# Performance work log

Measured on AMD Instinct MI355X. Metric: run time of the kernel, lower is better.

Reference implementation:

```python
import jax, jax.numpy as jnp
import numpy as np

B, L, D = 8, 2048, 1024
NH = 16            # n_head
HD = D // NH       # 64; attention is (HD x HD) per token in this module


def setup_inputs() -> dict:
    key = jax.random.key(0)
    ks = jax.random.split(key, 5)
    s = 0.02  # init scale for weights
    return {
        "x": jax.random.normal(ks[0], (B, L, D), jnp.float32),
        "Wq": jax.random.normal(ks[1], (D, D), jnp.float32) * s,
        "bq": jnp.zeros((D,), jnp.float32),
        "Wk": jax.random.normal(ks[2], (D, D), jnp.float32) * s,
        "bk": jnp.zeros((D,), jnp.float32),
        "Wv": jax.random.normal(ks[3], (D, D), jnp.float32) * s,
        "bv": jnp.zeros((D,), jnp.float32),
        "Wo": jax.random.normal(ks[4], (D, D), jnp.float32) * s,
        "bo": jnp.zeros((D,), jnp.float32),
    }


def reference(x, Wq, bq, Wk, bk, Wv, bv, Wo, bo):
    b, l, d = x.shape
    # QKV projections
    q = (x @ Wq + bq).reshape(b, l, HD, NH)
    k = (x @ Wk + bk).reshape(b, l, HD, NH)
    v = (x @ Wv + bv).reshape(b, l, HD, NH)
    # NOTE: module reshapes to (b, l, head_dim, n_head), so scores are
    # per-token (HD, HD) with the NH axis contracted; norm = sqrt(NH).
    norm = jnp.sqrt(jnp.asarray(NH, x.dtype))
    attn = jnp.einsum('blij,blkj->blik', q, k) / norm  # (b, l, HD, HD)
    attn = attn + 1e-06
    # mask = tril of the VALUES; jnp.where uses nonzero-as-True semantics.
    mask = jnp.tril(attn)
    attn = jnp.where(mask, attn, -jnp.inf)
    probs = jax.nn.softmax(attn, axis=-1)
    y = jnp.einsum('blik,blkj->blij', probs, v).reshape(b, l, d)
    return y @ Wo + bo
```

## Files before the change

### kernel.cpp

```cpp
#include <hip/hip_runtime.h>
#include <hip/hip_bf16.h>
#include <stdint.h>

typedef unsigned short u16;

#define Bdim 8
#define Ldim 2048
#define Ddim 1024
#define NH 16
#define HD 64
#define MTOK (Bdim*Ldim)

typedef __bf16 bf16x8 __attribute__((ext_vector_type(8)));
typedef float  f32x4  __attribute__((ext_vector_type(4)));
typedef float  f32x16 __attribute__((ext_vector_type(16)));

#define AS1 __attribute__((address_space(1)))
#define AS3 __attribute__((address_space(3)))

__device__ __forceinline__ void gload_lds16(const void* g, void* l) {
  __builtin_amdgcn_global_load_lds((const AS1 void*)g, (AS3 void*)l, 16, 0, 0);
}

__device__ __forceinline__ u16 f2bf(float f) {
  uint32_t u = __builtin_bit_cast(uint32_t, f);
  u += 0x7fffu + ((u >> 16) & 1u);
  return (u16)(u >> 16);
}
__device__ __forceinline__ uint32_t pkpair(float lo, float hi) {
  return (uint32_t)f2bf(lo) | ((uint32_t)f2bf(hi) << 16);
}

__global__ __launch_bounds__(256) void conv_f32_bf16(const float* __restrict__ in,
                                                     u16* __restrict__ out, int n4) {
  int i = blockIdx.x * 256 + threadIdx.x;
  if (i < n4) {
    float4 v = ((const float4*)in)[i];
    uint32_t w0 = (uint32_t)f2bf(v.x) | ((uint32_t)f2bf(v.y) << 16);
    uint32_t w1 = (uint32_t)f2bf(v.z) | ((uint32_t)f2bf(v.w) << 16);
    ((uint2*)out)[i] = make_uint2(w0, w1);
  }
}

__global__ __launch_bounds__(256) void conv_transpose_w(const float* __restrict__ W,
                                                        u16* __restrict__ Wt) {
  __shared__ float t[32][33];
  int tx = threadIdx.x & 31, ty = threadIdx.x >> 5;
  int k0 = blockIdx.x * 32, n0 = blockIdx.y * 32;
  #pragma unroll
  for (int i = 0; i < 32; i += 8)
    t[ty + i][tx] = W[(size_t)(k0 + ty + i) * Ddim + n0 + tx];
  __syncthreads();
  #pragma unroll
  for (int i = 0; i < 32; i += 8)
    Wt[(size_t)(n0 + ty + i) * Ddim + k0 + tx] = f2bf(t[tx][ty + i]);
}

template <int FUSED>
__global__ __launch_bounds__(512, 2) void gemm256(const u16* __restrict__ A,
                                                  const u16* __restrict__ Bt,
                                                  const float* __restrict__ b0p,
                                                  const float* __restrict__ b1p,
                                                  const float* __restrict__ b2p,
                                                  void* __restrict__ o0,
                                                  void* __restrict__ o1,
                                                  void* __restrict__ o2) {
  __shared__ alignas(16) u16 LP[65536];
  u16* LA = LP;
  u16* LB = LP + 32768;

  const int tid = threadIdx.x;
  const int wid = tid >> 6, lane = tid & 63;
  const int wr = wid >> 2, wc = wid & 3;
  const int fr = lane & 15, fh = lane >> 4;
  const int key = fr & 7;

  const int bid = blockIdx.x;
  const int xcd = bid & 7, idx = bid >> 3;
  const int mt = xcd * 8 + (idx & 7);
  const int nt = idx >> 3;
  const int m0 = mt * 256;
  const int n0g = nt * 256;

  const int srow = wid * 8 + (lane >> 3);
  const int scol = ((lane & 7) ^ (lane >> 3)) * 8;
  const u16* aG = A  + (size_t)(m0  + srow) * 1024 + scol;
  const u16* bG = Bt + (size_t)(n0g + srow) * 1024 + scol;
  const int ldsW = wid * 512;

#define STAGE(tile, buf) do {                                                  \
    const u16* ag_ = aG + (size_t)(tile) * 64;                                  \
    const u16* bg_ = bG + (size_t)(tile) * 64;                                  \
    _Pragma("unroll")                                                           \
    for (int s_ = 0; s_ < 4; ++s_) {                                            \
      gload_lds16(ag_ + (size_t)s_ * 65536, LA + (buf) * 16384 + s_ * 4096 + ldsW); \
      gload_lds16(bg_ + (size_t)s_ * 65536, LB + (buf) * 16384 + s_ * 4096 + ldsW); \
    }                                                                           \
  } while (0)

  f32x4 acc[8][4] = {};

#define COMPUTE(buf) do {                                                       \
    _Pragma("unroll")                                                           \
    for (int ks_ = 0; ks_ < 2; ++ks_) {                                         \
      bf16x8 af_[8], bf_[4];                                                    \
      const int p_ = ((ks_ * 4 + fh) ^ key) * 8;                                \
      _Pragma("unroll")                                                         \
      for (int m_ = 0; m_ < 8; ++m_)                                            \
        af_[m_] = *(const bf16x8*)(LA + (buf) * 16384 +                         \
                                   (wr * 128 + m_ * 16 + fr) * 64 + p_);        \
      _Pragma("unroll")                                                         \
      for (int n_ = 0; n_ < 4; ++n_)                                            \
        bf_[n_] = *(const bf16x8*)(LB + (buf) * 16384 +                         \
                                   (wc * 64 + n_ * 16 + fr) * 64 + p_);         \
      __builtin_amdgcn_s_setprio(1);                                            \
      _Pragma("unroll")                                                         \
      for (int m_ = 0; m_ < 8; ++m_)                                            \
        _Pragma("unroll")                                                       \
        for (int n_ = 0; n_ < 4; ++n_)                                          \
          acc[m_][n_] = __builtin_amdgcn_mfma_f32_16x16x32_bf16(                \
              af_[m_], bf_[n_], acc[m_][n_], 0, 0, 0);                          \
      __builtin_amdgcn_s_setprio(0);                                            \
    }                                                                           \
  } while (0)

  STAGE(0, 0);
  #pragma unroll 1
  for (int t = 0; t < 15; ++t) {
    const int cur = t & 1;
    STAGE(t + 1, cur ^ 1);
    asm volatile("s_waitcnt vmcnt(8)" ::: "memory");
    __builtin_amdgcn_s_barrier();
    COMPUTE(cur);
    asm volatile("s_waitcnt lgkmcnt(0)" ::: "memory");
    __builtin_amdgcn_s_barrier();
  }
  asm volatile("s_waitcnt vmcnt(0)" ::: "memory");
  __builtin_amdgcn_s_barrier();
  COMPUTE(1);
  __syncthreads();

  if (FUSED) {
    const int which = nt >> 2;
    const int n0l = (nt & 3) * 256;
    const float* bias = which == 0 ? b0p : which == 1 ? b1p : b2p;
    u16* Out = (u16*)(which == 0 ? o0 : which == 1 ? o1 : o2);
    u16* Ct = LP;
    #pragma unroll 1
    for (int h = 0; h < 2; ++h) {
      if (h) __syncthreads();
      if (wr == h) {
        #pragma unroll
        for (int n = 0; n < 4; ++n) {
          float bvv = bias[n0l + wc * 64 + n * 16 + fr];
          #pragma unroll
          for (int m = 0; m < 8; ++m)
            #pragma unroll
            for (int r = 0; r < 4; ++r)
              Ct[wc * 9216 + (m * 16 + fh * 4 + r) * 72 + n * 16 + fr] =
                  f2bf(acc[m][n][r] + bvv);
        }
      }
      __syncthreads();
      if (which != 2) {
        #pragma unroll
        for (int j = 0; j < 8; ++j) {
          int r = j * 16 + (tid >> 5), c8 = tid & 31;
          uint4 v = *(const uint4*)(Ct + (c8 >> 3) * 9216 + r * 72 + (c8 & 7) * 8);
          *(uint4*)(Out + (size_t)(m0 + h * 128 + r) * Ddim + n0l + c8 * 8) = v;
        }
      } else {
        #pragma unroll
        for (int j = 0; j < 4; ++j) {
          int q = j * 512 + tid, r = q >> 4, i = q & 15;
          u16 tmp[16];
          #pragma unroll
          for (int jj = 0; jj < 16; ++jj) {
            int c = i + 16 * jj;
            tmp[jj] = Ct[(c >> 6) * 9216 + r * 72 + (c & 63)];
          }
          u16* dst = Out + (size_t)(m0 + h * 128 + r) * Ddim + i * 64 + (n0l >> 4);
          *(uint4*)dst = *(uint4*)tmp;
          *(uint4*)(dst + 8) = *(uint4*)(tmp + 8);
        }
      }
      __syncthreads();
    }
  } else {
    float* Cf = (float*)LP;
    float* Out = (float*)o0;
    #pragma unroll 1
    for (int h = 0; h < 4; ++h) {
      if (h) __syncthreads();
      if (wr == (h >> 1) && (wc >> 1) == (h & 1)) {
        #pragma unroll
        for (int n = 0; n < 4; ++n) {
          int col = (wc & 1) * 64 + n * 16 + fr;
          float bvv = b0p[n0g + (h & 1) * 128 + col];
          #pragma unroll
          for (int m = 0; m < 8; ++m)
            #pragma unroll
            for (int r = 0; r < 4; ++r)
              Cf[(wc & 1) * 8704 + (m * 16 + fh * 4 + r) * 68 + n * 16 + fr] =
                  acc[m][n][r] + bvv;
        }
      }
      __syncthreads();
      #pragma unroll
      for (int j = 0; j < 8; ++j) {
        int r = j * 16 + (tid >> 5), c4 = tid & 31;
        float4 v = *(const float4*)(Cf + (c4 >> 4) * 8704 + r * 68 + (c4 & 15) * 4);
        *(float4*)(Out + (size_t)(m0 + (h >> 1) * 128 + r) * Ddim +
                   n0g + (h & 1) * 128 + c4 * 4) = v;
      }
      __syncthreads();
    }
  }
#undef STAGE
#undef COMPUTE
}

__global__ __launch_bounds__(256) void attn_mfma(const u16* __restrict__ Q,
                                                 const u16* __restrict__ Kb,
                                                 const u16* __restrict__ Vt,
                                                 u16* __restrict__ Y) {
  const int wid = threadIdx.x >> 6, lane = threadIdx.x & 63;
  const int tok = blockIdx.x * 4 + wid;
  const size_t base = (size_t)tok * Ddim;
  const int hi = lane >> 5, c31 = lane & 31;

  const bf16x8 kf0 = *(const bf16x8*)(Kb + base + (size_t)c31 * NH + hi * 8);
  const bf16x8 kf1 = *(const bf16x8*)(Kb + base + (size_t)(32 + c31) * NH + hi * 8);
  const bf16x8 qf0 = *(const bf16x8*)(Q  + base + (size_t)c31 * NH + hi * 8);
  const bf16x8 qf1 = *(const bf16x8*)(Q  + base + (size_t)(32 + c31) * NH + hi * 8);
  bf16x8 bv[4];
  #pragma unroll
  for (int c = 0; c < 4; ++c)
    bv[c] = *(const bf16x8*)(Vt + base + (size_t)(lane & 15) * HD + c * 16 + hi * 8);

  const f32x16 z = {};
  f32x16 s00 = __builtin_amdgcn_mfma_f32_32x32x16_bf16(kf0, qf0, z, 0, 0, 0);
  f32x16 s01 = __builtin_amdgcn_mfma_f32_32x32x16_bf16(kf0, qf1, z, 0, 0, 0);
  f32x16 s11 = __builtin_amdgcn_mfma_f32_32x32x16_bf16(kf1, qf1, z, 0, 0, 0);

  float a[16], b0[16], b1[16];
  float mA = -3e38f, mB = -3e38f;
  #pragma unroll
  for (int r = 0; r < 16; ++r) {
    const int kl = (r & 3) + 8 * (r >> 2) + 4 * hi;
    const bool keep = kl <= c31;
    float v00 = fmaf(s00[r], 0.25f, 1e-6f);
    float v01 = fmaf(s01[r], 0.25f, 1e-6f);
    float v11 = fmaf(s11[r], 0.25f, 1e-6f);
    a[r]  = keep ? v00 : -3e38f;
    b0[r] = v01;
    b1[r] = keep ? v11 : -3e38f;
    mA = fmaxf(mA, a[r]);
    mB = fmaxf(mB, fmaxf(b0[r], b1[r]));
  }
  mA = fmaxf(mA, __shfl_xor(mA, 32, 64));
  mB = fmaxf(mB, __shfl_xor(mB, 32, 64));
  float sA = 0.f, sB = 0.f;
  #pragma unroll
  for (int r = 0; r < 16; ++r) {
    a[r]  = __expf(a[r]  - mA);  sA += a[r];
    b0[r] = __expf(b0[r] - mB);
    b1[r] = __expf(b1[r] - mB);  sB += b0[r] + b1[r];
  }
  sA += __shfl_xor(sA, 32, 64);
  sB += __shfl_xor(sB, 32, 64);
  const float iA = __builtin_amdgcn_rcpf(sA);
  const float iB = __builtin_amdgcn_rcpf(sB);

  uint32_t pA[4][2], pB0[4][2], pB1[4][2];
  #pragma unroll
  for (int m = 0; m < 4; ++m)
    #pragma unroll
    for (int t = 0; t < 2; ++t) {
      pA [m][t] = pkpair(a [4*m+2*t] * iA, a [4*m+2*t+1] * iA);
      pB0[m][t] = pkpair(b0[4*m+2*t] * iB, b0[4*m+2*t+1] * iB);
      pB1[m][t] = pkpair(b1[4*m+2*t] * iB, b1[4*m+2*t+1] * iB);
    }

#define AFRAG(dst, src, cp) do {                                              \
    uint32_t k0_ = hi ? src[2*(cp)+1][0] : src[2*(cp)][0];                    \
    uint32_t k1_ = hi ? src[2*(cp)+1][1] : src[2*(cp)][1];                    \
    uint32_t s0_ = hi ? src[2*(cp)][0]   : src[2*(cp)+1][0];                  \
    uint32_t s1_ = hi ? src[2*(cp)][1]   : src[2*(cp)+1][1];                  \
    uint32_t r0_ = (uint32_t)__shfl_xor((int)s0_, 32, 64);                    \
    uint32_t r1_ = (uint32_t)__shfl_xor((int)s1_, 32, 64);                    \
    union { uint32_t w[4]; bf16x8 v; } u_;                                    \
    u_.w[0] = hi ? r0_ : k0_;  u_.w[1] = hi ? r1_ : k1_;                      \
    u_.w[2] = hi ? k0_ : r0_;  u_.w[3] = hi ? k1_ : r1_;                      \
    dst = u_.v;                                                               \
  } while (0)

  f32x16 y0 = {}, y1 = {};
  bf16x8 af;
  AFRAG(af, pA, 0);  y0 = __builtin_amdgcn_mfma_f32_32x32x16_bf16(af, bv[0], y0, 0, 0, 0);
  AFRAG(af, pA, 1);  y0 = __builtin_amdgcn_mfma_f32_32x32x16_bf16(af, bv[1], y0, 0, 0, 0);
  AFRAG(af, pB0, 0); y1 = __builtin_amdgcn_mfma_f32_32x32x16_bf16(af, bv[0], y1, 0, 0, 0);
  AFRAG(af, pB0, 1); y1 = __builtin_amdgcn_mfma_f32_32x32x16_bf16(af, bv[1], y1, 0, 0, 0);
  AFRAG(af, pB1, 0); y1 = __builtin_amdgcn_mfma_f32_32x32x16_bf16(af, bv[2], y1, 0, 0, 0);
  AFRAG(af, pB1, 1); y1 = __builtin_amdgcn_mfma_f32_32x32x16_bf16(af, bv[3], y1, 0, 0, 0);
#undef AFRAG

  if (c31 < 16) {
    #pragma unroll
    for (int r = 0; r < 16; ++r) {
      const int row = (r & 3) + 8 * (r >> 2) + 4 * hi;
      Y[base + (size_t)row * NH + c31]        = f2bf(y0[r]);
      Y[base + (size_t)(32 + row) * NH + c31] = f2bf(y1[r]);
    }
  }
}

extern "C" void kernel_launch(void* const* d_in, const int* in_sizes, int n_in,
                              void* d_out, int out_size, void* d_ws, size_t ws_size,
                              hipStream_t stream) {
  const float* x  = (const float*)d_in[0];
  const float* Wq = (const float*)d_in[1];
  const float* bq = (const float*)d_in[2];
  const float* Wk = (const float*)d_in[3];
  const float* bk = (const float*)d_in[4];
  const float* Wv = (const float*)d_in[5];
  const float* bv = (const float*)d_in[6];
  const float* Wo = (const float*)d_in[7];
  const float* bo = (const float*)d_in[8];
  float* out = (float*)d_out;

  u16* xb = (u16*)d_ws;
  u16* Wt = xb + (size_t)MTOK * Ddim;
  u16* Qb = Wt + 4ull * Ddim * Ddim;
  u16* Kb = Qb + (size_t)MTOK * Ddim;
  u16* Vb = Kb + (size_t)MTOK * Ddim;
  u16* Yb = xb;

  conv_f32_bf16<<<(MTOK * Ddim / 4 + 255) / 256, 256, 0, stream>>>(x, xb, MTOK * Ddim / 4);

  dim3 tg(Ddim / 32, Ddim / 32);
  conv_transpose_w<<<tg, 256, 0, stream>>>(Wq, Wt + 0ull * Ddim * Ddim);
  conv_transpose_w<<<tg, 256, 0, stream>>>(Wk, Wt + 1ull * Ddim * Ddim);
  conv_transpose_w<<<tg, 256, 0, stream>>>(Wv, Wt + 2ull * Ddim * Ddim);
  conv_transpose_w<<<tg, 256, 0, stream>>>(Wo, Wt + 3ull * Ddim * Ddim);

  gemm256<1><<<dim3(768), 512, 0, stream>>>(xb, Wt, bq, bk, bv, Qb, Kb, Vb);

  attn_mfma<<<MTOK / 4, 256, 0, stream>>>(Qb, Kb, Vb, Yb);

  gemm256<0><<<dim3(256), 512, 0, stream>>>(Yb, Wt + 3ull * Ddim * Ddim,
                                            bo, bo, bo, out, out, out);
}
```

Baseline: 213.3 us.

## Interleave global-to-LDS loads, LDS fragment reads and MFMAs in GEMM main loop

Restructures the GEMM K-loop into four quarter-steps that alternate between two register fragment sets. Each quarter-step issues part of the next tile's global-to-LDS loads, prefetches LDS fragments for the next MFMA group and runs 16 MFMAs, so loads, LDS reads and matrix math overlap within a tile. The old version ran a full stage-wait-compute-barrier cycle per tile. The new schedule adds more barriers and finer vmcnt waits, and it raises register pressure from the extra fragment buffers.

```diff
diff --git a/kernel.cpp b/kernel.cpp
--- a/kernel.cpp
+++ b/kernel.cpp
@@ -88,56 +88,75 @@
   const u16* bG = Bt + (size_t)(n0g + srow) * 1024 + scol;
   const int ldsW = wid * 512;
 
-#define STAGE(tile, buf) do {                                                  \
-    const u16* ag_ = aG + (size_t)(tile) * 64;                                  \
-    const u16* bg_ = bG + (size_t)(tile) * 64;                                  \
+#define STG(MAT, S_, TILE, BUF)                                                 \
+  gload_lds16(((MAT) ? bG : aG) + (size_t)(TILE) * 64 + (size_t)(S_) * 65536,   \
+              ((MAT) ? LB : LA) + (BUF) * 16384 + (S_) * 4096 + ldsW)
+
+#define RD_AF(DST, BUF, KS, MH) do {                                            \
+    const u16* base_ = LA + (BUF) * 16384;                                      \
+    const int p_ = (((KS) * 4 + fh) ^ key) * 8;                                 \
     _Pragma("unroll")                                                           \
-    for (int s_ = 0; s_ < 4; ++s_) {                                            \
-      gload_lds16(ag_ + (size_t)s_ * 65536, LA + (buf) * 16384 + s_ * 4096 + ldsW); \
-      gload_lds16(bg_ + (size_t)s_ * 65536, LB + (buf) * 16384 + s_ * 4096 + ldsW); \
-    }                                                                           \
+    for (int mm_ = 0; mm_ < 4; ++mm_)                                           \
+      DST[mm_] = *(const bf16x8*)(base_ +                                       \
+                   (wr * 128 + (MH) * 64 + mm_ * 16 + fr) * 64 + p_);           \
   } while (0)
-
-  f32x4 acc[8][4] = {};
-
-#define COMPUTE(buf) do {                                                       \
+#define RD_BF(DST, BUF, KS) do {                                                \
+    const u16* base_ = LB + (BUF) * 16384;                                      \
+    const int p_ = (((KS) * 4 + fh) ^ key) * 8;                                 \
     _Pragma("unroll")                                                           \
-    for (int ks_ = 0; ks_ < 2; ++ks_) {                                         \
-      bf16x8 af_[8], bf_[4];                                                    \
-      const int p_ = ((ks_ * 4 + fh) ^ key) * 8;                                \
-      _Pragma("unroll")                                                         \
-      for (int m_ = 0; m_ < 8; ++m_)                                            \
-        af_[m_] = *(const bf16x8*)(LA + (buf) * 16384 +                         \
-                                   (wr * 128 + m_ * 16 + fr) * 64 + p_);        \
+    for (int n_ = 0; n_ < 4; ++n_)                                              \
+      DST[n_] = *(const bf16x8*)(base_ + (wc * 64 + n_ * 16 + fr) * 64 + p_);   \
+  } while (0)
+#define MFMA16(AF, BF, MH) do {                                                 \
+    __builtin_amdgcn_s_setprio(1);                                              \
+    _Pragma("unroll")                                                           \
+    for (int mm_ = 0; mm_ < 4; ++mm_)                                           \
       _Pragma("unroll")                                                         \
       for (int n_ = 0; n_ < 4; ++n_)                                            \
-        bf_[n_] = *(const bf16x8*)(LB + (buf) * 16384 +                         \
-                                   (wc * 64 + n_ * 16 + fr) * 64 + p_);         \
-      __builtin_amdgcn_s_setprio(1);                                            \
-      _Pragma("unroll")                                                         \
-      for (int m_ = 0; m_ < 8; ++m_)                                            \
-        _Pragma("unroll")                                                       \
-        for (int n_ = 0; n_ < 4; ++n_)                                          \
-          acc[m_][n_] = __builtin_amdgcn_mfma_f32_16x16x32_bf16(                \
-              af_[m_], bf_[n_], acc[m_][n_], 0, 0, 0);                          \
-      __builtin_amdgcn_s_setprio(0);                                            \
-    }                                                                           \
+        acc[(MH) * 4 + mm_][n_] = __builtin_amdgcn_mfma_f32_16x16x32_bf16(      \
+            AF[mm_], BF[n_], acc[(MH) * 4 + mm_][n_], 0, 0, 0);                 \
+    __builtin_amdgcn_s_setprio(0);                                              \
   } while (0)
-
-  STAGE(0, 0);
+#define WAITV(N) asm volatile("s_waitcnt vmcnt(" #N ")" ::: "memory")
+#define BAR() __builtin_amdgcn_s_barrier()
+
+  f32x4 acc[8][4] = {};
+  bf16x8 afA[4], afB[4], bf0[4], bf1[4];
+
+  STG(1,0,0,0); STG(1,1,0,0); STG(1,2,0,0); STG(1,3,0,0);
+  STG(0,0,0,0); STG(0,2,0,0); STG(0,1,0,0); STG(0,3,0,0);
+  WAITV(2); BAR();
+  RD_AF(afA, 0, 0, 0); RD_BF(bf0, 0, 0);
+
   #pragma unroll 1
   for (int t = 0; t < 15; ++t) {
-    const int cur = t & 1;
-    STAGE(t + 1, cur ^ 1);
-    asm volatile("s_waitcnt vmcnt(8)" ::: "memory");
-    __builtin_amdgcn_s_barrier();
-    COMPUTE(cur);
-    asm volatile("s_waitcnt lgkmcnt(0)" ::: "memory");
-    __builtin_amdgcn_s_barrier();
-  }
-  asm volatile("s_waitcnt vmcnt(0)" ::: "memory");
-  __builtin_amdgcn_s_barrier();
-  COMPUTE(1);
+    const int cur = t & 1, nxt = cur ^ 1;
+    STG(1,0,t+1,nxt); STG(1,1,t+1,nxt);
+    BAR();
+    RD_AF(afB, cur, 1, 0); RD_BF(bf1, cur, 1);
+    MFMA16(afA, bf0, 0);
+    STG(1,2,t+1,nxt); STG(1,3,t+1,nxt);
+    WAITV(4); BAR();
+    RD_AF(afA, cur, 0, 1);
+    MFMA16(afB, bf1, 0);
+    STG(0,0,t+1,nxt); STG(0,2,t+1,nxt);
+    BAR();
+    RD_AF(afB, cur, 1, 1);
+    MFMA16(afA, bf0, 1);
+    STG(0,1,t+1,nxt); STG(0,3,t+1,nxt);
+    WAITV(2); BAR();
+    RD_AF(afA, nxt, 0, 0); RD_BF(bf0, nxt, 0);
+    MFMA16(afB, bf1, 1);
+  }
+  RD_AF(afB, 1, 1, 0); RD_BF(bf1, 1, 1);
+  MFMA16(afA, bf0, 0);
+  WAITV(0); BAR();
+  RD_AF(afA, 1, 0, 1);
+  MFMA16(afB, bf1, 0);
+  RD_AF(afB, 1, 1, 1);
+  MFMA16(afA, bf0, 1);
+  MFMA16(afB, bf1, 1);
+
   __syncthreads();
 
   if (FUSED) {
@@ -195,8 +214,7 @@
       if (wr == (h >> 1) && (wc >> 1) == (h & 1)) {
         #pragma unroll
         for (int n = 0; n < 4; ++n) {
-          int col = (wc & 1) * 64 + n * 16 + fr;
-          float bvv = b0p[n0g + (h & 1) * 128 + col];
+          float bvv = b0p[n0g + (h & 1) * 128 + (wc & 1) * 64 + n * 16 + fr];
           #pragma unroll
           for (int m = 0; m < 8; ++m)
             #pragma unroll
@@ -216,8 +234,12 @@
       __syncthreads();
     }
   }
-#undef STAGE
-#undef COMPUTE
+#undef STG
+#undef RD_AF
+#undef RD_BF
+#undef MFMA16
+#undef WAITV
+#undef BAR
 }
 
 __global__ __launch_bounds__(256) void attn_mfma(const u16* __restrict__ Q,
```

Measured after the change: 206.9 us. 1.03x faster.

## Restructure GEMM main loop into 8-phase interleaved load/compute pipeline

Applied to the files above, without the earlier changes.

Replaces the double-buffered stage/compute loop in the bf16 GEMM with an 8-phase schedule. Each phase splits the tile into half-tiles, interleaves LDS fragment reads, global-to-LDS half-tile loads and a 16-MFMA cluster, and puts barriers between them. The aim is to hide LDS read latency and global load latency behind MFMA work, in the style of ping-pong GEMM schedules. It adds many more barriers and fine-grained vmcnt waits, so correctness depends on the hand-tracked buffer and ordering logic.

```diff
diff --git a/kernel.cpp b/kernel.cpp
--- a/kernel.cpp
+++ b/kernel.cpp
@@ -57,87 +57,103 @@
 }
 
 template <int FUSED>
-__global__ __launch_bounds__(512, 2) void gemm256(const u16* __restrict__ A,
-                                                  const u16* __restrict__ Bt,
-                                                  const float* __restrict__ b0p,
-                                                  const float* __restrict__ b1p,
-                                                  const float* __restrict__ b2p,
-                                                  void* __restrict__ o0,
-                                                  void* __restrict__ o1,
-                                                  void* __restrict__ o2) {
+__global__ __launch_bounds__(512, 2) void gemm8p(const u16* __restrict__ A,
+                                                 const u16* __restrict__ Bt,
+                                                 const float* __restrict__ b0p,
+                                                 const float* __restrict__ b1p,
+                                                 const float* __restrict__ b2p,
+                                                 void* __restrict__ o0,
+                                                 void* __restrict__ o1,
+                                                 void* __restrict__ o2) {
   __shared__ alignas(16) u16 LP[65536];
-  u16* LA = LP;
-  u16* LB = LP + 32768;
-
   const int tid = threadIdx.x;
   const int wid = tid >> 6, lane = tid & 63;
   const int wr = wid >> 2, wc = wid & 3;
   const int fr = lane & 15, fh = lane >> 4;
-  const int key = fr & 7;
 
   const int bid = blockIdx.x;
   const int xcd = bid & 7, idx = bid >> 3;
   const int mt = xcd * 8 + (idx & 7);
   const int nt = idx >> 3;
-  const int m0 = mt * 256;
-  const int n0g = nt * 256;
-
-  const int srow = wid * 8 + (lane >> 3);
-  const int scol = ((lane & 7) ^ (lane >> 3)) * 8;
-  const u16* aG = A  + (size_t)(m0  + srow) * 1024 + scol;
-  const u16* bG = Bt + (size_t)(n0g + srow) * 1024 + scol;
-  const int ldsW = wid * 512;
-
-#define STAGE(tile, buf) do {                                                  \
-    const u16* ag_ = aG + (size_t)(tile) * 64;                                  \
-    const u16* bg_ = bG + (size_t)(tile) * 64;                                  \
-    _Pragma("unroll")                                                           \
-    for (int s_ = 0; s_ < 4; ++s_) {                                            \
-      gload_lds16(ag_ + (size_t)s_ * 65536, LA + (buf) * 16384 + s_ * 4096 + ldsW); \
-      gload_lds16(bg_ + (size_t)s_ * 65536, LB + (buf) * 16384 + s_ * 4096 + ldsW); \
-    }                                                                           \
-  } while (0)
+  const int m0 = mt * 256, n0g = nt * 256;
+
+  const int x7 = fr & 7;
+  const int cks0 = (fh ^ x7) * 8;
+  const int cks1 = ((4 + fh) ^ x7) * 8;
+  const int rA = (wr * 128 + fr) * 64;
+  const int rB = (wc * 64 + fr) * 64;
+
+  const int srt = tid >> 3;
+  const int sgc = ((tid & 7) ^ (srt & 7)) * 8;
+  const u16* aSt = A  + (size_t)(m0  + srt) * 1024 + sgc;
+  const u16* bSt = Bt + (size_t)(n0g + srt) * 1024 + sgc;
+
+#define RDA4(DST, B_, KS_, MH_) do {                                           \
+    const u16* p_ = LP + (B_) * 16384 + rA + (MH_) * 4096 + ((KS_) ? cks1 : cks0); \
+    DST[0] = *(const bf16x8*)(p_);                                             \
+    DST[1] = *(const bf16x8*)(p_ + 1024);                                      \
+    DST[2] = *(const bf16x8*)(p_ + 2048);                                      \
+    DST[3] = *(const bf16x8*)(p_ + 3072);                                      \
+  } while (0)
+#define RDB4(DST, B_, KS_) do {                                                \
+    const u16* p_ = LP + 32768 + (B_) * 16384 + rB + ((KS_) ? cks1 : cks0);    \
+    DST[0] = *(const bf16x8*)(p_);                                             \
+    DST[1] = *(const bf16x8*)(p_ + 1024);                                      \
+    DST[2] = *(const bf16x8*)(p_ + 2048);                                      \
+    DST[3] = *(const bf16x8*)(p_ + 3072);                                      \
+  } while (0)
+#define STGH(ISB_, T_, H_, B_) do {                                            \
+    const u16* s_ = ((ISB_) ? bSt : aSt) + (size_t)(H_) * 131072 + (size_t)(T_) * 64; \
+    u16* d_ = (u16*)LP + ((ISB_) ? 32768 : 0) + (B_) * 16384 + (H_) * 8192 + (wid << 9); \
+    gload_lds16(s_, d_);                                                       \
+    gload_lds16(s_ + 65536, d_ + 4096);                                        \
+  } while (0)
+#define MFMA16(AF, BF, MH) do {                                                \
+    __builtin_amdgcn_s_setprio(1);                                             \
+    _Pragma("unroll")                                                          \
+    for (int mm_ = 0; mm_ < 4; ++mm_)                                          \
+      _Pragma("unroll")                                                        \
+      for (int n_ = 0; n_ < 4; ++n_)                                           \
+        acc[(MH) * 4 + mm_][n_] = __builtin_amdgcn_mfma_f32_16x16x32_bf16(     \
+            AF[mm_], BF[n_], acc[(MH) * 4 + mm_][n_], 0, 0, 0);                \
+    __builtin_amdgcn_s_setprio(0);                                             \
+  } while (0)
+#define WAITV(N) asm volatile("s_waitcnt vmcnt(" #N ")" ::: "memory")
+#define BAR() do { asm volatile("" ::: "memory");                              \
+                   __builtin_amdgcn_s_barrier();                               \
+                   asm volatile("" ::: "memory"); } while (0)
 
   f32x4 acc[8][4] = {};
-
-#define COMPUTE(buf) do {                                                       \
-    _Pragma("unroll")                                                           \
-    for (int ks_ = 0; ks_ < 2; ++ks_) {                                         \
-      bf16x8 af_[8], bf_[4];                                                    \
-      const int p_ = ((ks_ * 4 + fh) ^ key) * 8;                                \
-      _Pragma("unroll")                                                         \
-      for (int m_ = 0; m_ < 8; ++m_)                                            \
-        af_[m_] = *(const bf16x8*)(LA + (buf) * 16384 +                         \
-                                   (wr * 128 + m_ * 16 + fr) * 64 + p_);        \
-      _Pragma("unroll")                                                         \
-      for (int n_ = 0; n_ < 4; ++n_)                                            \
-        bf_[n_] = *(const bf16x8*)(LB + (buf) * 16384 +                         \
-                                   (wc * 64 + n_ * 16 + fr) * 64 + p_);         \
-      __builtin_amdgcn_s_setprio(1);                                            \
-      _Pragma("unroll")                                                         \
-      for (int m_ = 0; m_ < 8; ++m_)                                            \
-        _Pragma("unroll")                                                       \
-        for (int n_ = 0; n_ < 4; ++n_)                                          \
-          acc[m_][n_] = __builtin_amdgcn_mfma_f32_16x16x32_bf16(                \
-              af_[m_], bf_[n_], acc[m_][n_], 0, 0, 0);                          \
-      __builtin_amdgcn_s_setprio(0);                                            \
-    }                                                                           \
-  } while (0)
-
-  STAGE(0, 0);
+  bf16x8 aA[4], aB[4], bA[4], bB[4];
+
+  STGH(1, 0, 0, 0); STGH(0, 0, 0, 0); STGH(1, 0, 1, 0); STGH(0, 0, 1, 0);
+  STGH(1, 1, 0, 1); STGH(0, 1, 0, 1);
+  WAITV(4);
+  BAR();
+  RDA4(aA, 0, 0, 0); RDB4(bA, 0, 0);
+
   #pragma unroll 1
-  for (int t = 0; t < 15; ++t) {
-    const int cur = t & 1;
-    STAGE(t + 1, cur ^ 1);
-    asm volatile("s_waitcnt vmcnt(8)" ::: "memory");
-    __builtin_amdgcn_s_barrier();
-    COMPUTE(cur);
-    asm volatile("s_waitcnt lgkmcnt(0)" ::: "memory");
-    __builtin_amdgcn_s_barrier();
-  }
-  asm volatile("s_waitcnt vmcnt(0)" ::: "memory");
-  __builtin_amdgcn_s_barrier();
-  COMPUTE(1);
+  for (int i = 0; i < 8; ++i) {
+    const int u1 = 2 * i + 1;
+    const int s2 = (i < 7) ? 2 * i + 2 : 14;
+    const int s3 = (i < 7) ? 2 * i + 3 : 15;
+    RDA4(aB, 0, 0, 1);                 STGH(1, u1, 1, 1);
+    BAR(); MFMA16(aA, bA, 0); BAR();
+    RDA4(aA, 0, 1, 0); RDB4(bB, 0, 1); STGH(0, u1, 1, 1);
+    BAR(); MFMA16(aB, bA, 1); BAR();
+    RDA4(aB, 0, 1, 1);                 STGH(1, s2, 0, 0);
+    BAR(); MFMA16(aA, bB, 0); WAITV(2); BAR();
+    RDA4(aA, 1, 0, 0); RDB4(bA, 1, 0); STGH(0, s2, 0, 0);
+    BAR(); MFMA16(aB, bB, 1); BAR();
+    RDA4(aB, 1, 0, 1);                 STGH(1, s2, 1, 0);
+    BAR(); MFMA16(aA, bA, 0); BAR();
+    RDA4(aA, 1, 1, 0); RDB4(bB, 1, 1); STGH(0, s2, 1, 0);
+    BAR(); MFMA16(aB, bA, 1); BAR();
+    RDA4(aB, 1, 1, 1);                 STGH(1, s3, 0, 1);
+    BAR(); MFMA16(aA, bB, 0); WAITV(2); BAR();
+    RDA4(aA, 0, 0, 0); RDB4(bA, 0, 0); STGH(0, s3, 0, 1);
+    BAR(); MFMA16(aB, bB, 1); BAR();
+  }
   __syncthreads();
 
   if (FUSED) {
@@ -172,14 +188,14 @@
       } else {
         #pragma unroll
         for (int j = 0; j < 4; ++j) {
-          int q = j * 512 + tid, r = q >> 4, i = q & 15;
+          int q = j * 512 + tid, r = q >> 4, ii = q & 15;
           u16 tmp[16];
           #pragma unroll
           for (int jj = 0; jj < 16; ++jj) {
-            int c = i + 16 * jj;
+            int c = ii + 16 * jj;
             tmp[jj] = Ct[(c >> 6) * 9216 + r * 72 + (c & 63)];
           }
-          u16* dst = Out + (size_t)(m0 + h * 128 + r) * Ddim + i * 64 + (n0l >> 4);
+          u16* dst = Out + (size_t)(m0 + h * 128 + r) * Ddim + ii * 64 + (n0l >> 4);
           *(uint4*)dst = *(uint4*)tmp;
           *(uint4*)(dst + 8) = *(uint4*)(tmp + 8);
         }
@@ -195,8 +211,7 @@
       if (wr == (h >> 1) && (wc >> 1) == (h & 1)) {
         #pragma unroll
         for (int n = 0; n < 4; ++n) {
-          int col = (wc & 1) * 64 + n * 16 + fr;
-          float bvv = b0p[n0g + (h & 1) * 128 + col];
+          float bvv = b0p[n0g + (h & 1) * 128 + (wc & 1) * 64 + n * 16 + fr];
           #pragma unroll
           for (int m = 0; m < 8; ++m)
             #pragma unroll
@@ -216,8 +231,12 @@
       __syncthreads();
     }
   }
-#undef STAGE
-#undef COMPUTE
+#undef RDA4
+#undef RDB4
+#undef STGH
+#undef MFMA16
+#undef WAITV
+#undef BAR
 }
 
 __global__ __launch_bounds__(256) void attn_mfma(const u16* __restrict__ Q,
@@ -344,10 +363,10 @@
   conv_transpose_w<<<tg, 256, 0, stream>>>(Wv, Wt + 2ull * Ddim * Ddim);
   conv_transpose_w<<<tg, 256, 0, stream>>>(Wo, Wt + 3ull * Ddim * Ddim);
 
-  gemm256<1><<<dim3(768), 512, 0, stream>>>(xb, Wt, bq, bk, bv, Qb, Kb, Vb);
+  gemm8p<1><<<dim3(768), 512, 0, stream>>>(xb, Wt, bq, bk, bv, Qb, Kb, Vb);
 
   attn_mfma<<<MTOK / 4, 256, 0, stream>>>(Qb, Kb, Vb, Yb);
 
-  gemm256<0><<<dim3(256), 512, 0, stream>>>(Yb, Wt + 3ull * Ddim * Ddim,
-                                            bo, bo, bo, out, out, out);
-}
+  gemm8p<0><<<dim3(256), 512, 0, stream>>>(Yb, Wt + 3ull * Ddim * Ddim,
+                                           bo, bo, bo, out, out, out);
+}
```

Result: faster. 209.1 us (-2.0%).
